# Performance work log

Measured on AMD Instinct MI355X. Metric: run time of the kernel, lower is better.

The kernel has to match this reference:

```python
import jax, jax.numpy as jnp
import numpy as np

REF_CHANNEL = 0
DIAG_EPS = 1e-7   # diag_loading coefficient
TIK_EPS = 1e-8    # additive eps in diagonal loading / trace denominator
MASK_EPS = 1e-15  # PSD mask-normalization eps


def _psd(spec, mask):
    # spec: (b, c, f, t) complex; mask: (b, f, t) real
    # PSD module: normalize mask over time, weight outer products, sum over t.
    m = mask / (mask.sum(axis=-1, keepdims=True) + MASK_EPS)
    return jnp.einsum('bcft,beft,bft->bfce', spec, spec.conj(), m.astype(spec.dtype))


def setup_inputs() -> dict:
    key = jax.random.key(0)
    k1, k2, k3, k4 = jax.random.split(key, 4)
    B, C, F, T = 4, 6, 257, 2000
    return {
        'spec_real': jax.random.normal(k1, (B, C, F, T), dtype=jnp.float32),
        'spec_imag': jax.random.normal(k2, (B, C, F, T), dtype=jnp.float32),
        'mask_s': jax.random.uniform(k3, (B, F, T), dtype=jnp.float32),
        'mask_n': jax.random.uniform(k4, (B, F, T), dtype=jnp.float32),
    }


def reference(spec_real, spec_imag, mask_s, mask_n):
    spec = spec_real + 1j * spec_imag                     # (b, c, f, t) complex64
    C = spec.shape[1]

    psd_s = _psd(spec, mask_s)                            # (b, f, c, c)
    psd_n = _psd(spec, mask_n)                            # (b, f, c, c)

    # Diagonal loading (Tikhonov regularization) of the noise PSD.
    tr_n = jnp.einsum('bfcc->bf', psd_n).real
    epsilon = jax.lax.stop_gradient(tr_n * DIAG_EPS + TIK_EPS)   # torch uses no_grad here
    psd_n = psd_n + epsilon[..., None, None] * jnp.eye(C, dtype=spec.dtype)

    # ref_channel solution: w = (psd_n^-1 psd_s) / trace(psd_n^-1 psd_s) @ u
    numerator = jnp.linalg.solve(psd_n, psd_s)            # (b, f, c, c)
    tr = jnp.einsum('bfcc->bf', numerator)
    ws = numerator / (tr[..., None, None] + TIK_EPS)
    w = ws[..., :, REF_CHANNEL]                           # one-hot u selects column -> (b, f, c)

    # enhanced = w^H Y
    enh = jnp.einsum('bfc,bcft->bft', w.conj(), spec)     # (b, f, t) complex
    return jnp.stack([enh.real, enh.imag], axis=-1)       # (b, f, t, 2) float32
```

## Files before the change

kernel.cpp:

```cpp
#include <hip/hip_runtime.h>

#define NB 4
#define NC 6
#define NF 257
#define NT 2000
#define NG (NB * NF)
#define NPAIR 15
#define NACC 74
#define BLK 256
#define NP2 (NT / 2)
#define NJ 4
#define CS  (NF * NT)
#define CS2 (CS / 2)

typedef float nfloat4 __attribute__((ext_vector_type(4)));

template<int CTRL>
__device__ __forceinline__ float dpp_add(float v) {
    int s = __builtin_amdgcn_update_dpp(0, __builtin_bit_cast(int, v), CTRL, 0xF, 0xF, true);
    return v + __builtin_bit_cast(float, s);
}

__device__ __forceinline__ int qidx(int c, int e) {
    return c * (2 * NC - 1 - c) / 2 + (e - c - 1);
}

__global__ __launch_bounds__(BLK) void mvdr_fused(
    const float* __restrict__ sr, const float* __restrict__ si,
    const float* __restrict__ ms, const float* __restrict__ mn,
    float* __restrict__ out)
{
    constexpr int PC[NPAIR] = {0,0,0,0,0,1,1,1,1,2,2,2,3,3,4};
    constexpr int PE[NPAIR] = {1,2,3,4,5,2,3,4,5,3,4,5,4,5,5};

    const int g  = blockIdx.x;
    const int b  = g / NF;
    const int f  = g - b * NF;
    const int sbase = b * NC * CS + f * NT;
    const int mbase = g * NT;
    const int tid = threadIdx.x;

    const float2* s2r = (const float2*)(sr + sbase);
    const float2* s2i = (const float2*)(si + sbase);
    const float2* m2s = (const float2*)(ms + mbase);
    const float2* m2n = (const float2*)(mn + mbase);

    float acc[NACC];
    #pragma unroll
    for (int i = 0; i < NACC; i++) acc[i] = 0.f;

    #pragma unroll
    for (int j = 0; j < NJ; j++) {
        const int q0 = j * BLK + tid;
        const bool act = q0 < NP2;
        const int p = act ? q0 : 0;
        float wms[2], wmn[2], rr[NC][2], ii[NC][2];
        {
            const float2 t0 = m2s[p];
            wms[0] = t0.x; wms[1] = t0.y;
            const float2 t1 = m2n[p];
            wmn[0] = t1.x; wmn[1] = t1.y;
        }
        #pragma unroll
        for (int c = 0; c < NC; c++) {
            const float2 tr = s2r[c * CS2 + p];
            rr[c][0] = tr.x; rr[c][1] = tr.y;
            const float2 ti = s2i[c * CS2 + p];
            ii[c][0] = ti.x; ii[c][1] = ti.y;
        }
        if (!act) { wms[0] = wms[1] = wmn[0] = wmn[1] = 0.f; }
        #pragma unroll
        for (int k = 0; k < 2; k++) { acc[72] += wms[k]; acc[73] += wmn[k]; }
        #pragma unroll
        for (int c = 0; c < NC; c++) {
            #pragma unroll
            for (int k = 0; k < 2; k++) {
                const float d = rr[c][k] * rr[c][k] + ii[c][k] * ii[c][k];
                acc[c]     += d * wms[k];
                acc[6 + c] += d * wmn[k];
            }
        }
        #pragma unroll
        for (int q = 0; q < NPAIR; q++) {
            const int c = PC[q], e = PE[q];
            #pragma unroll
            for (int k = 0; k < 2; k++) {
                const float cr = rr[c][k] * rr[e][k] + ii[c][k] * ii[e][k];
                const float ci = ii[c][k] * rr[e][k] - rr[c][k] * ii[e][k];
                acc[12 + 4 * q + 0] += cr * wms[k];
                acc[12 + 4 * q + 1] += ci * wms[k];
                acc[12 + 4 * q + 2] += cr * wmn[k];
                acc[12 + 4 * q + 3] += ci * wmn[k];
            }
        }
    }

    #pragma unroll
    for (int i = 0; i < NACC; i++) {
        float v = acc[i];
        v = dpp_add<0x118>(v);
        v = dpp_add<0x114>(v);
        v = dpp_add<0x112>(v);
        acc[i] = v;
    }

    __shared__ float red[32][NACC];
    __shared__ float fin[NACC];
    __shared__ float sdr[NC], sdi[NC];
    __shared__ float wsh[2 * NC];

    const int lane16 = tid & 15;
    const int ridx   = ((tid >> 4) << 1) | (lane16 & 1);
    if (lane16 >= 14) {
        #pragma unroll
        for (int i = 0; i < NACC; i++) red[ridx][i] = acc[i];
    }
    __syncthreads();

    if (tid < NACC) {
        float s = 0.f;
        #pragma unroll
        for (int r = 0; r < 32; r++) s += red[r][tid];
        fin[tid] = s;
    }
    __syncthreads();

    float xr[NC], xi[NC];
    if (tid < NC) {
        const float invS = 1.f / (fin[72] + 1e-15f);
        const float invN = 1.f / (fin[73] + 1e-15f);

        float Ar[NC][NC], Ai[NC][NC];
        #pragma unroll
        for (int c = 0; c < NC; c++) { Ar[c][c] = fin[6 + c] * invN; Ai[c][c] = 0.f; }
        #pragma unroll
        for (int q = 0; q < NPAIR; q++) {
            const int c = PC[q], e = PE[q];
            const float nre = fin[12 + 4 * q + 2] * invN;
            const float nim = fin[12 + 4 * q + 3] * invN;
            Ar[c][e] = nre;  Ai[c][e] = nim;
            Ar[e][c] = nre;  Ai[e][c] = -nim;
        }
        {
            float trn = 0.f;
            #pragma unroll
            for (int c = 0; c < NC; c++) trn += Ar[c][c];
            const float eps = trn * 1e-7f + 1e-8f;
            #pragma unroll
            for (int c = 0; c < NC; c++) Ar[c][c] += eps;
        }

        #pragma unroll
        for (int k = 0; k < NC; k++) {
            const float dr = Ar[k][k], di = Ai[k][k];
            const float idn = 1.f / (dr * dr + di * di);
            const float pr = dr * idn, pi = -di * idn;
            #pragma unroll
            for (int i = k + 1; i < NC; i++) {
                const float lr = Ar[i][k] * pr - Ai[i][k] * pi;
                const float li = Ar[i][k] * pi + Ai[i][k] * pr;
                Ar[i][k] = lr; Ai[i][k] = li;
                #pragma unroll
                for (int j = k + 1; j < NC; j++) {
                    Ar[i][j] -= lr * Ar[k][j] - li * Ai[k][j];
                    Ai[i][j] -= lr * Ai[k][j] + li * Ar[k][j];
                }
            }
        }

        #pragma unroll
        for (int i = 0; i < NC; i++) {
            if (i == tid)      { xr[i] = fin[i] * invS;  xi[i] = 0.f; }
            else if (i < tid)  { const int q = qidx(i, tid);
                                 xr[i] = fin[12 + 4 * q] * invS;  xi[i] =  fin[13 + 4 * q] * invS; }
            else               { const int q = qidx(tid, i);
                                 xr[i] = fin[12 + 4 * q] * invS;  xi[i] = -fin[13 + 4 * q] * invS; }
        }
        #pragma unroll
        for (int i = 1; i < NC; i++) {
            #pragma unroll
            for (int k = 0; k < NC - 1; k++) if (k < i) {
                xr[i] -= Ar[i][k] * xr[k] - Ai[i][k] * xi[k];
                xi[i] -= Ar[i][k] * xi[k] + Ai[i][k] * xr[k];
            }
        }
        #pragma unroll
        for (int i = NC - 1; i >= 0; i--) {
            #pragma unroll
            for (int k = 0; k < NC; k++) if (k > i) {
                xr[i] -= Ar[i][k] * xr[k] - Ai[i][k] * xi[k];
                xi[i] -= Ar[i][k] * xi[k] + Ai[i][k] * xr[k];
            }
            const float dr = Ar[i][i], di = Ai[i][i];
            const float idn = 1.f / (dr * dr + di * di);
            const float pr = dr * idn, pi = -di * idn;
            const float t0 = xr[i] * pr - xi[i] * pi;
            xi[i] = xr[i] * pi + xi[i] * pr;
            xr[i] = t0;
        }
        float dgr = xr[0], dgi = xi[0];
        #pragma unroll
        for (int i = 1; i < NC; i++) if (tid == i) { dgr = xr[i]; dgi = xi[i]; }
        sdr[tid] = dgr; sdi[tid] = dgi;
    }
    __syncthreads();

    if (tid == 0) {
        float trr = 1e-8f, tri = 0.f;
        #pragma unroll
        for (int c = 0; c < NC; c++) { trr += sdr[c]; tri += sdi[c]; }
        const float idn = 1.f / (trr * trr + tri * tri);
        #pragma unroll
        for (int c = 0; c < NC; c++) {
            const float wre = (xr[c] * trr + xi[c] * tri) * idn;
            const float wim = (xi[c] * trr - xr[c] * tri) * idn;
            wsh[c]      = wre;
            wsh[6 + c]  = -wim;
        }
    }
    __syncthreads();

    float wr[NC], wi[NC];
    #pragma unroll
    for (int c = 0; c < NC; c++) { wr[c] = wsh[c]; wi[c] = wsh[6 + c]; }

    nfloat4* o4 = (nfloat4*)(out + 2 * mbase);
    #pragma unroll
    for (int j = 0; j < NJ; j++) {
        const int p = j * BLK + tid;
        if (p < NP2) {
            float rr[NC][2], ii[NC][2];
            #pragma unroll
            for (int c = 0; c < NC; c++) {
                const float2 tr = s2r[c * CS2 + p];
                rr[c][0] = tr.x; rr[c][1] = tr.y;
                const float2 ti = s2i[c * CS2 + p];
                ii[c][0] = ti.x; ii[c][1] = ti.y;
            }
            float er[2], ei[2];
            #pragma unroll
            for (int k = 0; k < 2; k++) {
                float a = 0.f, bb = 0.f;
                #pragma unroll
                for (int c = 0; c < NC; c++) {
                    a  += wr[c] * rr[c][k] - wi[c] * ii[c][k];
                    bb += wr[c] * ii[c][k] + wi[c] * rr[c][k];
                }
                er[k] = a; ei[k] = bb;
            }
            nfloat4 o0 = {er[0], ei[0], er[1], ei[1]};
            __builtin_nontemporal_store(o0, &o4[p]);
        }
    }
}

extern "C" void kernel_launch(void* const* d_in, const int* in_sizes, int n_in,
                              void* d_out, int out_size, void* d_ws, size_t ws_size,
                              hipStream_t stream) {
    const float* sr = (const float*)d_in[0];
    const float* si = (const float*)d_in[1];
    const float* ms = (const float*)d_in[2];
    const float* mn = (const float*)d_in[3];
    float* out = (float*)d_out;
    (void)d_ws; (void)ws_size;

    mvdr_fused<<<NG, BLK, 0, stream>>>(sr, si, ms, mn, out);
}
```

Before: 176.7 us.

## Split fused MVDR kernel into chunked PSD and solve-apply kernels

Splits the single fused kernel, which used one block per (b,f), into two kernels that each use four blocks per (b,f), one per time chunk. The PSD kernel writes partial accumulators to workspace. The solve/apply kernel sums the four partials, redoes the 6x6 solve redundantly in each chunk block, and applies the beamformer to its own chunk. The goal is more blocks for better occupancy and latency hiding, at the cost of an extra launch, a workspace round trip, and the solve being repeated four times per (b,f).

```diff
diff --git a/kernel.cpp b/kernel.cpp
--- a/kernel.cpp
+++ b/kernel.cpp
@@ -7,9 +7,10 @@
 #define NG (NB * NF)
 #define NPAIR 15
 #define NACC 74
+#define NCHUNK 4
+#define TCH (NT / NCHUNK)
+#define NP2 (TCH / 2)
 #define BLK 256
-#define NP2 (NT / 2)
-#define NJ 4
 #define CS  (NF * NT)
 #define CS2 (CS / 2)
 
@@ -25,20 +26,21 @@
     return c * (2 * NC - 1 - c) / 2 + (e - c - 1);
 }
 
-__global__ __launch_bounds__(BLK) void mvdr_fused(
+__global__ __launch_bounds__(BLK) void psd_kernel(
     const float* __restrict__ sr, const float* __restrict__ si,
     const float* __restrict__ ms, const float* __restrict__ mn,
-    float* __restrict__ out)
+    float* __restrict__ wsp)
 {
     constexpr int PC[NPAIR] = {0,0,0,0,0,1,1,1,1,2,2,2,3,3,4};
     constexpr int PE[NPAIR] = {1,2,3,4,5,2,3,4,5,3,4,5,4,5,5};
 
-    const int g  = blockIdx.x;
+    const int bx = blockIdx.x;
+    const int g  = bx >> 2;
     const int b  = g / NF;
     const int f  = g - b * NF;
-    const int sbase = b * NC * CS + f * NT;
-    const int mbase = g * NT;
-    const int tid = threadIdx.x;
+    const int tb = (bx & 3) * TCH;
+    const int sbase = b * NC * CS + f * NT + tb;
+    const int mbase = g * NT + tb;
 
     const float2* s2r = (const float2*)(sr + sbase);
     const float2* s2i = (const float2*)(si + sbase);
@@ -49,11 +51,9 @@
     #pragma unroll
     for (int i = 0; i < NACC; i++) acc[i] = 0.f;
 
-    #pragma unroll
-    for (int j = 0; j < NJ; j++) {
-        const int q0 = j * BLK + tid;
-        const bool act = q0 < NP2;
-        const int p = act ? q0 : 0;
+    const bool act = threadIdx.x < NP2;
+    const int  p   = act ? threadIdx.x : 0;
+    {
         float wms[2], wmn[2], rr[NC][2], ii[NC][2];
         {
             const float2 t0 = m2s[p];
@@ -105,23 +105,44 @@
     }
 
     __shared__ float red[32][NACC];
+    const int lane16 = threadIdx.x & 15;
+    const int ridx   = ((threadIdx.x >> 4) << 1) | (lane16 & 1);
+    if (lane16 >= 14) {
+        #pragma unroll
+        for (int i = 0; i < NACC; i++) red[ridx][i] = acc[i];
+    }
+    __syncthreads();
+
+    if (threadIdx.x < NACC) {
+        float s = 0.f;
+        #pragma unroll
+        for (int r = 0; r < 32; r++) s += red[r][threadIdx.x];
+        wsp[bx * NACC + threadIdx.x] = s;
+    }
+}
+
+__global__ __launch_bounds__(BLK) void solve_apply_kernel(
+    const float* __restrict__ sr, const float* __restrict__ si,
+    const float* __restrict__ wsp, float* __restrict__ out)
+{
+    constexpr int PC[NPAIR] = {0,0,0,0,0,1,1,1,1,2,2,2,3,3,4};
+    constexpr int PE[NPAIR] = {1,2,3,4,5,2,3,4,5,3,4,5,4,5,5};
+
+    const int bx = blockIdx.x;
+    const int g  = bx >> 2;
+    const int b  = g / NF;
+    const int f  = g - b * NF;
+    const int tb = (bx & 3) * TCH;
+    const int sbase = b * NC * CS + f * NT + tb;
+    const int tid = threadIdx.x;
+
     __shared__ float fin[NACC];
     __shared__ float sdr[NC], sdi[NC];
     __shared__ float wsh[2 * NC];
 
-    const int lane16 = tid & 15;
-    const int ridx   = ((tid >> 4) << 1) | (lane16 & 1);
-    if (lane16 >= 14) {
-        #pragma unroll
-        for (int i = 0; i < NACC; i++) red[ridx][i] = acc[i];
-    }
-    __syncthreads();
-
+    const float* p0 = wsp + (4 * g) * NACC;
     if (tid < NACC) {
-        float s = 0.f;
-        #pragma unroll
-        for (int r = 0; r < 32; r++) s += red[r][tid];
-        fin[tid] = s;
+        fin[tid] = (p0[tid] + p0[NACC + tid]) + (p0[2 * NACC + tid] + p0[3 * NACC + tid]);
     }
     __syncthreads();
 
@@ -214,8 +235,8 @@
         for (int c = 0; c < NC; c++) {
             const float wre = (xr[c] * trr + xi[c] * tri) * idn;
             const float wim = (xi[c] * trr - xr[c] * tri) * idn;
-            wsh[c]      = wre;
-            wsh[6 + c]  = -wim;
+            wsh[c]     = wre;
+            wsh[6 + c] = -wim;
         }
     }
     __syncthreads();
@@ -224,33 +245,33 @@
     #pragma unroll
     for (int c = 0; c < NC; c++) { wr[c] = wsh[c]; wi[c] = wsh[6 + c]; }
 
-    nfloat4* o4 = (nfloat4*)(out + 2 * mbase);
-    #pragma unroll
-    for (int j = 0; j < NJ; j++) {
-        const int p = j * BLK + tid;
-        if (p < NP2) {
-            float rr[NC][2], ii[NC][2];
+    const float2* s2r = (const float2*)(sr + sbase);
+    const float2* s2i = (const float2*)(si + sbase);
+    nfloat4* o4 = (nfloat4*)(out + 2 * (g * NT + tb));
+
+    const int p = tid;
+    if (p < NP2) {
+        float rr[NC][2], ii[NC][2];
+        #pragma unroll
+        for (int c = 0; c < NC; c++) {
+            const float2 tr = s2r[c * CS2 + p];
+            rr[c][0] = tr.x; rr[c][1] = tr.y;
+            const float2 ti = s2i[c * CS2 + p];
+            ii[c][0] = ti.x; ii[c][1] = ti.y;
+        }
+        float er[2], ei[2];
+        #pragma unroll
+        for (int k = 0; k < 2; k++) {
+            float a = 0.f, bb = 0.f;
             #pragma unroll
             for (int c = 0; c < NC; c++) {
-                const float2 tr = s2r[c * CS2 + p];
-                rr[c][0] = tr.x; rr[c][1] = tr.y;
-                const float2 ti = s2i[c * CS2 + p];
-                ii[c][0] = ti.x; ii[c][1] = ti.y;
-            }
-            float er[2], ei[2];
-            #pragma unroll
-            for (int k = 0; k < 2; k++) {
-                float a = 0.f, bb = 0.f;
-                #pragma unroll
-                for (int c = 0; c < NC; c++) {
-                    a  += wr[c] * rr[c][k] - wi[c] * ii[c][k];
-                    bb += wr[c] * ii[c][k] + wi[c] * rr[c][k];
-                }
-                er[k] = a; ei[k] = bb;
-            }
-            nfloat4 o0 = {er[0], ei[0], er[1], ei[1]};
-            __builtin_nontemporal_store(o0, &o4[p]);
-        }
+                a  += wr[c] * rr[c][k] - wi[c] * ii[c][k];
+                bb += wr[c] * ii[c][k] + wi[c] * rr[c][k];
+            }
+            er[k] = a; ei[k] = bb;
+        }
+        nfloat4 o0 = {er[0], ei[0], er[1], ei[1]};
+        __builtin_nontemporal_store(o0, &o4[p]);
     }
 }
 
@@ -262,7 +283,9 @@
     const float* ms = (const float*)d_in[2];
     const float* mn = (const float*)d_in[3];
     float* out = (float*)d_out;
-    (void)d_ws; (void)ws_size;
-
-    mvdr_fused<<<NG, BLK, 0, stream>>>(sr, si, ms, mn, out);
-}
+
+    float* wsp = (float*)d_ws;
+
+    psd_kernel<<<NG * NCHUNK, BLK, 0, stream>>>(sr, si, ms, mn, wsp);
+    solve_apply_kernel<<<NG * NCHUNK, BLK, 0, stream>>>(sr, si, wsp, out);
+}
```

Result: faster. 170.7 us (-3.4%).

## Software-pipeline loads with double buffers and prefetch apply-phase data before reduction

Applied to the files above, without the earlier changes.

The accumulation loop becomes a two-buffer software pipeline, so the loads for the next time chunk are in flight while the current chunk is accumulated. The first two chunks of spec needed by the output phase are loaded before the cross-lane reduction and solve, hiding that latency behind the serial middle section. In exchange, register pressure rises (two P1 buffers plus two P3 buffers of 24 floats alongside 74 accumulators), which may lower occupancy or cause spills.

```diff
diff --git a/kernel.cpp b/kernel.cpp
--- a/kernel.cpp
+++ b/kernel.cpp
@@ -8,7 +8,7 @@
 #define NPAIR 15
 #define NACC 74
 #define BLK 256
-#define NP2 (NT / 2)
+#define NP2G (NT / 2)
 #define NJ 4
 #define CS  (NF * NT)
 #define CS2 (CS / 2)
@@ -24,6 +24,85 @@
 __device__ __forceinline__ int qidx(int c, int e) {
     return c * (2 * NC - 1 - c) / 2 + (e - c - 1);
 }
+
+struct P1Buf { float wms[2], wmn[2], rr[NC][2], ii[NC][2]; };
+struct P3Buf { float rr[NC][2], ii[NC][2]; };
+
+#define P1_LOAD(BUF, J) do {                                                   \
+    const int q0_ = (J) * BLK + tid;                                           \
+    const bool act_ = ((J) < 3) || (q0_ < NP2G);                               \
+    const int p_ = act_ ? q0_ : 0;                                             \
+    { const float2 t0_ = m2s[p_]; BUF.wms[0] = t0_.x; BUF.wms[1] = t0_.y; }    \
+    { const float2 t1_ = m2n[p_]; BUF.wmn[0] = t1_.x; BUF.wmn[1] = t1_.y; }    \
+    _Pragma("unroll")                                                          \
+    for (int c = 0; c < NC; c++) {                                             \
+        const float2 tr_ = s2r[c * CS2 + p_];                                  \
+        BUF.rr[c][0] = tr_.x; BUF.rr[c][1] = tr_.y;                            \
+        const float2 ti_ = s2i[c * CS2 + p_];                                  \
+        BUF.ii[c][0] = ti_.x; BUF.ii[c][1] = ti_.y;                            \
+    }                                                                          \
+    if (!act_) { BUF.wms[0] = BUF.wms[1] = BUF.wmn[0] = BUF.wmn[1] = 0.f; }    \
+} while (0)
+
+#define P1_ACC(BUF) do {                                                       \
+    _Pragma("unroll")                                                          \
+    for (int k = 0; k < 2; k++) { acc[72] += BUF.wms[k]; acc[73] += BUF.wmn[k]; } \
+    _Pragma("unroll")                                                          \
+    for (int c = 0; c < NC; c++) {                                             \
+        _Pragma("unroll")                                                      \
+        for (int k = 0; k < 2; k++) {                                          \
+            const float d_ = BUF.rr[c][k] * BUF.rr[c][k] + BUF.ii[c][k] * BUF.ii[c][k]; \
+            acc[c]     += d_ * BUF.wms[k];                                     \
+            acc[6 + c] += d_ * BUF.wmn[k];                                     \
+        }                                                                      \
+    }                                                                          \
+    _Pragma("unroll")                                                          \
+    for (int q = 0; q < NPAIR; q++) {                                          \
+        const int c_ = PC[q], e_ = PE[q];                                      \
+        _Pragma("unroll")                                                      \
+        for (int k = 0; k < 2; k++) {                                          \
+            const float cr_ = BUF.rr[c_][k] * BUF.rr[e_][k] + BUF.ii[c_][k] * BUF.ii[e_][k]; \
+            const float ci_ = BUF.ii[c_][k] * BUF.rr[e_][k] - BUF.rr[c_][k] * BUF.ii[e_][k]; \
+            acc[12 + 4 * q + 0] += cr_ * BUF.wms[k];                           \
+            acc[12 + 4 * q + 1] += ci_ * BUF.wms[k];                           \
+            acc[12 + 4 * q + 2] += cr_ * BUF.wmn[k];                           \
+            acc[12 + 4 * q + 3] += ci_ * BUF.wmn[k];                           \
+        }                                                                      \
+    }                                                                          \
+} while (0)
+
+#define P3_LOAD(BUF, J) do {                                                   \
+    const int q0_ = (J) * BLK + tid;                                           \
+    const bool act_ = ((J) < 3) || (q0_ < NP2G);                               \
+    const int p_ = act_ ? q0_ : 0;                                             \
+    _Pragma("unroll")                                                          \
+    for (int c = 0; c < NC; c++) {                                             \
+        const float2 tr_ = s2r[c * CS2 + p_];                                  \
+        BUF.rr[c][0] = tr_.x; BUF.rr[c][1] = tr_.y;                            \
+        const float2 ti_ = s2i[c * CS2 + p_];                                  \
+        BUF.ii[c][0] = ti_.x; BUF.ii[c][1] = ti_.y;                            \
+    }                                                                          \
+} while (0)
+
+#define P3_APPLY(BUF, J) do {                                                  \
+    const int q0_ = (J) * BLK + tid;                                           \
+    const bool act_ = ((J) < 3) || (q0_ < NP2G);                               \
+    float er_[2], ei_[2];                                                      \
+    _Pragma("unroll")                                                          \
+    for (int k = 0; k < 2; k++) {                                              \
+        float a_ = 0.f, b_ = 0.f;                                              \
+        _Pragma("unroll")                                                      \
+        for (int c = 0; c < NC; c++) {                                         \
+            a_ += wr[c] * BUF.rr[c][k] - wi[c] * BUF.ii[c][k];                 \
+            b_ += wr[c] * BUF.ii[c][k] + wi[c] * BUF.rr[c][k];                 \
+        }                                                                      \
+        er_[k] = a_; ei_[k] = b_;                                              \
+    }                                                                          \
+    if (act_) {                                                                \
+        nfloat4 o0_ = {er_[0], ei_[0], er_[1], ei_[1]};                        \
+        __builtin_nontemporal_store(o0_, &o4[q0_]);                            \
+    }                                                                          \
+} while (0)
 
 __global__ __launch_bounds__(BLK) void mvdr_fused(
     const float* __restrict__ sr, const float* __restrict__ si,
@@ -37,63 +116,32 @@
     const int b  = g / NF;
     const int f  = g - b * NF;
     const int sbase = b * NC * CS + f * NT;
-    const int mbase = g * NT;
     const int tid = threadIdx.x;
 
     const float2* s2r = (const float2*)(sr + sbase);
     const float2* s2i = (const float2*)(si + sbase);
-    const float2* m2s = (const float2*)(ms + mbase);
-    const float2* m2n = (const float2*)(mn + mbase);
+    const float2* m2s = (const float2*)(ms + g * NT);
+    const float2* m2n = (const float2*)(mn + g * NT);
 
     float acc[NACC];
     #pragma unroll
     for (int i = 0; i < NACC; i++) acc[i] = 0.f;
 
-    #pragma unroll
-    for (int j = 0; j < NJ; j++) {
-        const int q0 = j * BLK + tid;
-        const bool act = q0 < NP2;
-        const int p = act ? q0 : 0;
-        float wms[2], wmn[2], rr[NC][2], ii[NC][2];
-        {
-            const float2 t0 = m2s[p];
-            wms[0] = t0.x; wms[1] = t0.y;
-            const float2 t1 = m2n[p];
-            wmn[0] = t1.x; wmn[1] = t1.y;
-        }
-        #pragma unroll
-        for (int c = 0; c < NC; c++) {
-            const float2 tr = s2r[c * CS2 + p];
-            rr[c][0] = tr.x; rr[c][1] = tr.y;
-            const float2 ti = s2i[c * CS2 + p];
-            ii[c][0] = ti.x; ii[c][1] = ti.y;
-        }
-        if (!act) { wms[0] = wms[1] = wmn[0] = wmn[1] = 0.f; }
-        #pragma unroll
-        for (int k = 0; k < 2; k++) { acc[72] += wms[k]; acc[73] += wmn[k]; }
-        #pragma unroll
-        for (int c = 0; c < NC; c++) {
-            #pragma unroll
-            for (int k = 0; k < 2; k++) {
-                const float d = rr[c][k] * rr[c][k] + ii[c][k] * ii[c][k];
-                acc[c]     += d * wms[k];
-                acc[6 + c] += d * wmn[k];
-            }
-        }
-        #pragma unroll
-        for (int q = 0; q < NPAIR; q++) {
-            const int c = PC[q], e = PE[q];
-            #pragma unroll
-            for (int k = 0; k < 2; k++) {
-                const float cr = rr[c][k] * rr[e][k] + ii[c][k] * ii[e][k];
-                const float ci = ii[c][k] * rr[e][k] - rr[c][k] * ii[e][k];
-                acc[12 + 4 * q + 0] += cr * wms[k];
-                acc[12 + 4 * q + 1] += ci * wms[k];
-                acc[12 + 4 * q + 2] += cr * wmn[k];
-                acc[12 + 4 * q + 3] += ci * wmn[k];
-            }
-        }
-    }
+    {
+        P1Buf A, B;
+        P1_LOAD(A, 0);
+        P1_LOAD(B, 1);
+        P1_ACC(A);
+        P1_LOAD(A, 2);
+        P1_ACC(B);
+        P1_LOAD(B, 3);
+        P1_ACC(A);
+        P1_ACC(B);
+    }
+
+    P3Buf PA, PB;
+    P3_LOAD(PA, 0);
+    P3_LOAD(PB, 1);
 
     #pragma unroll
     for (int i = 0; i < NACC; i++) {
@@ -214,8 +262,8 @@
         for (int c = 0; c < NC; c++) {
             const float wre = (xr[c] * trr + xi[c] * tri) * idn;
             const float wim = (xi[c] * trr - xr[c] * tri) * idn;
-            wsh[c]      = wre;
-            wsh[6 + c]  = -wim;
+            wsh[c]     = wre;
+            wsh[6 + c] = -wim;
         }
     }
     __syncthreads();
@@ -224,34 +272,14 @@
     #pragma unroll
     for (int c = 0; c < NC; c++) { wr[c] = wsh[c]; wi[c] = wsh[6 + c]; }
 
-    nfloat4* o4 = (nfloat4*)(out + 2 * mbase);
-    #pragma unroll
-    for (int j = 0; j < NJ; j++) {
-        const int p = j * BLK + tid;
-        if (p < NP2) {
-            float rr[NC][2], ii[NC][2];
-            #pragma unroll
-            for (int c = 0; c < NC; c++) {
-                const float2 tr = s2r[c * CS2 + p];
-                rr[c][0] = tr.x; rr[c][1] = tr.y;
-                const float2 ti = s2i[c * CS2 + p];
-                ii[c][0] = ti.x; ii[c][1] = ti.y;
-            }
-            float er[2], ei[2];
-            #pragma unroll
-            for (int k = 0; k < 2; k++) {
-                float a = 0.f, bb = 0.f;
-                #pragma unroll
-                for (int c = 0; c < NC; c++) {
-                    a  += wr[c] * rr[c][k] - wi[c] * ii[c][k];
-                    bb += wr[c] * ii[c][k] + wi[c] * rr[c][k];
-                }
-                er[k] = a; ei[k] = bb;
-            }
-            nfloat4 o0 = {er[0], ei[0], er[1], ei[1]};
-            __builtin_nontemporal_store(o0, &o4[p]);
-        }
-    }
+    nfloat4* o4 = (nfloat4*)(out + 2 * g * NT);
+
+    P3_APPLY(PA, 0);
+    P3_LOAD(PA, 2);
+    P3_APPLY(PB, 1);
+    P3_LOAD(PB, 3);
+    P3_APPLY(PA, 2);
+    P3_APPLY(PB, 3);
 }
 
 extern "C" void kernel_launch(void* const* d_in, const int* in_sizes, int n_in,
```

Measured after the change: 175.8 us. About the same (-0.5%).
